# Performance work log

Hardware: AMD Instinct MI355X
Metric: run time of the kernel (lower is better)

## Reference

```python
import jax, jax.numpy as jnp
import numpy as np

NUM_LEVELS = 16
MIN_RES = 16
GROWTH = 1.38
TABLE_SZ = 16384
# Per-level resolutions computed in float64 like torch's python-float b**level
RESOLUTIONS = jnp.asarray(np.floor(MIN_RES * GROWTH ** np.arange(NUM_LEVELS)).astype(np.float32))
# Spatial-hash constants; 2654435761 wraps to int32 like torch's .int() arithmetic
H2 = np.uint32(2654435761).astype(np.int32)
H3 = np.int32(805459861)
# Corner order v0..v7 from get_nearest_vertices_coords: 1 -> use ceil, 0 -> use floor
CORNERS = np.array([[0,0,0],[1,0,0],[1,1,0],[0,1,0],[0,0,1],[1,0,1],[1,1,1],[0,1,1]], dtype=bool)


def setup_inputs() -> dict:
    key = jax.random.key(0)
    kx, kt = jax.random.split(key)
    x = jax.random.uniform(kx, (262144, 3), dtype=jnp.float32)
    # original init: uniform(-1e-4, 1e-4); small-scale random values
    tables = jax.random.normal(kt, (NUM_LEVELS, TABLE_SZ, 2), dtype=jnp.float32) * 1e-4
    return {"x": x, "tables": tables}


def reference(x, tables):
    B = x.shape[0]
    F = tables.shape[-1]
    mask = jnp.asarray(CORNERS)  # [8,3]
    scaled = RESOLUTIONS[:, None, None] * x[None]        # [L,B,3]
    lo = jnp.floor(scaled).astype(jnp.int32)             # [L,B,3]
    hi = jnp.ceil(scaled).astype(jnp.int32)              # [L,B,3]
    verts = jnp.where(mask[None, None], hi[:, :, None, :], lo[:, :, None, :])  # [L,B,8,3]
    vx, vy, vz = verts[..., 0], verts[..., 1], verts[..., 2]
    # int32 spatial hash with wraparound multiply, then python-style mod (non-negative)
    idx = jnp.remainder(vx ^ (H2 * vy) ^ (H3 * vz), TABLE_SZ)  # [L,B,8]
    feats = jax.vmap(lambda t, i: t[i])(tables, idx)           # [L,B,8,F]
    # NOTE: faithful to source: interpolation weights use the UNSCALED position
    w = x - jnp.floor(x)                                       # [B,3]
    # trilinear weight per corner = prod_d (w_d if corner high else 1-w_d)
    cw = jnp.prod(jnp.where(mask[None], w[:, None, :], 1.0 - w[:, None, :]), axis=-1)  # [B,8]
    out = jnp.einsum('lbvf,bv->lbf', feats, cw)                # [L,B,F]
    return jnp.transpose(out, (1, 0, 2)).reshape(B, NUM_LEVELS * F)
```

## Files before the change

### kernel.cpp

```cpp
#include <hip/hip_runtime.h>
#include <hip/hip_fp16.h>
#include <stdint.h>


#define NUM_LEVELS 16
#define TABLE_SZ   16384
#define NCHUNK     32
#define BLOCK      1024

__constant__ float RESV[NUM_LEVELS] = {
    16.f, 22.f, 30.f, 42.f, 58.f, 80.f, 110.f, 152.f,
    210.f, 290.f, 400.f, 553.f, 763.f, 1053.f, 1453.f, 2005.f
};

#define H2_LO 14769u
#define H3_LO 6037u

#define COMPUTE(PX,PY,PZ, OXY0,OXY1,OXY2,OXY3,MZL,MZH, W0,W1,W2,W3,OZ,WZ)      \
    {                                                                          \
        float wx_ = (PX) - floorf(PX);                                         \
        float wy_ = (PY) - floorf(PY);                                         \
        float wz_ = (PZ) - floorf(PZ);                                         \
        float ox_ = 1.f - wx_, oy_ = 1.f - wy_;                                \
        OZ = 1.f - wz_; WZ = wz_;                                              \
        W0 = ox_ * oy_; W1 = wx_ * oy_; W2 = wx_ * wy_; W3 = ox_ * wy_;        \
        float sx_ = r * (PX), sy_ = r * (PY), sz_ = r * (PZ);                  \
        uint32_t mxl_ = ((uint32_t)(int)floorf(sx_) & (TABLE_SZ - 1)) << 2;    \
        uint32_t mxh_ = ((uint32_t)(int)ceilf(sx_)  & (TABLE_SZ - 1)) << 2;    \
        uint32_t myl_ = (__umul24(H2_LO, (uint32_t)(int)floorf(sy_))           \
                         & (TABLE_SZ - 1)) << 2;                               \
        uint32_t myh_ = (__umul24(H2_LO, (uint32_t)(int)ceilf(sy_))            \
                         & (TABLE_SZ - 1)) << 2;                               \
        MZL = (__umul24(H3_LO, (uint32_t)(int)floorf(sz_))                     \
               & (TABLE_SZ - 1)) << 2;                                         \
        MZH = (__umul24(H3_LO, (uint32_t)(int)ceilf(sz_))                      \
               & (TABLE_SZ - 1)) << 2;                                         \
        OXY0 = mxl_ ^ myl_; OXY1 = mxh_ ^ myl_;                                \
        OXY2 = mxh_ ^ myh_; OXY3 = mxl_ ^ myh_;                                \
    }

__global__ __launch_bounds__(BLOCK, 8)
void hashenc_lds_kernel(const float* __restrict__ x,
                        const float* __restrict__ tables,
                        float* __restrict__ out,
                        int B, int pts_per_block)
{
    __shared__ __half2 tab[TABLE_SZ];

    const int level = blockIdx.x >> 5;
    const int chunk = blockIdx.x & (NCHUNK - 1);

    {
        const float4* __restrict__ gt4 =
            (const float4*)(tables + (size_t)level * (TABLE_SZ * 2));
        #pragma unroll
        for (int i = threadIdx.x; i < TABLE_SZ / 2; i += BLOCK) {
            float4 v = gt4[i];
            tab[2 * i]     = __floats2half2_rn(v.x, v.y);
            tab[2 * i + 1] = __floats2half2_rn(v.z, v.w);
        }
    }
    __syncthreads();

    const float r = RESV[level];
    const int b0 = chunk * pts_per_block + threadIdx.x;
    const int iters = pts_per_block / BLOCK;

    const float* __restrict__ xp = x + 3 * (size_t)b0;
    const float* __restrict__ xf = xp + 3 * 2 * BLOCK;
    float2* __restrict__ op = (float2*)out + (size_t)b0 * NUM_LEVELS + level;
    const char* tb = (const char*)tab;

    float px = xp[0], py = xp[1], pz = xp[2];
    uint32_t c_oxy0, c_oxy1, c_oxy2, c_oxy3, c_mzl, c_mzh;
    float    c_w0, c_w1, c_w2, c_w3, c_oz, c_wz;
    COMPUTE(px, py, pz, c_oxy0, c_oxy1, c_oxy2, c_oxy3, c_mzl, c_mzh,
            c_w0, c_w1, c_w2, c_w3, c_oz, c_wz);

    float nx = px, ny = py, nz = pz;
    if (iters > 1) {
        nx = xp[3 * BLOCK + 0];
        ny = xp[3 * BLOCK + 1];
        nz = xp[3 * BLOCK + 2];
    }

    #pragma unroll 1
    for (int k = 0; k < iters; ++k) {
        __half2 h0 = *(const __half2*)(tb + (c_oxy0 ^ c_mzl));
        __half2 h1 = *(const __half2*)(tb + (c_oxy1 ^ c_mzl));
        __half2 h2 = *(const __half2*)(tb + (c_oxy2 ^ c_mzl));
        __half2 h3 = *(const __half2*)(tb + (c_oxy3 ^ c_mzl));
        __half2 h4 = *(const __half2*)(tb + (c_oxy0 ^ c_mzh));
        __half2 h5 = *(const __half2*)(tb + (c_oxy1 ^ c_mzh));
        __half2 h6 = *(const __half2*)(tb + (c_oxy2 ^ c_mzh));
        __half2 h7 = *(const __half2*)(tb + (c_oxy3 ^ c_mzh));

        float fx = nx, fy = ny, fz = nz;
        if (k + 2 < iters) {
            nx = xf[0]; ny = xf[1]; nz = xf[2];
        }
        xf += 3 * BLOCK;

        uint32_t n_oxy0, n_oxy1, n_oxy2, n_oxy3, n_mzl, n_mzh;
        float    n_w0, n_w1, n_w2, n_w3, n_oz, n_wz;
        COMPUTE(fx, fy, fz, n_oxy0, n_oxy1, n_oxy2, n_oxy3, n_mzl, n_mzh,
                n_w0, n_w1, n_w2, n_w3, n_oz, n_wz);

        float a0 = 0.f, a1 = 0.f;
        {
            float w0 = c_w0 * c_oz, w1 = c_w1 * c_oz,
                  w2 = c_w2 * c_oz, w3 = c_w3 * c_oz;
            a0 = fmaf(__low2float(h0),  w0, a0);
            a1 = fmaf(__high2float(h0), w0, a1);
            a0 = fmaf(__low2float(h1),  w1, a0);
            a1 = fmaf(__high2float(h1), w1, a1);
            a0 = fmaf(__low2float(h2),  w2, a0);
            a1 = fmaf(__high2float(h2), w2, a1);
            a0 = fmaf(__low2float(h3),  w3, a0);
            a1 = fmaf(__high2float(h3), w3, a1);
        }
        {
            float w0 = c_w0 * c_wz, w1 = c_w1 * c_wz,
                  w2 = c_w2 * c_wz, w3 = c_w3 * c_wz;
            a0 = fmaf(__low2float(h4),  w0, a0);
            a1 = fmaf(__high2float(h4), w0, a1);
            a0 = fmaf(__low2float(h5),  w1, a0);
            a1 = fmaf(__high2float(h5), w1, a1);
            a0 = fmaf(__low2float(h6),  w2, a0);
            a1 = fmaf(__high2float(h6), w2, a1);
            a0 = fmaf(__low2float(h7),  w3, a0);
            a1 = fmaf(__high2float(h7), w3, a1);
        }

        *op = make_float2(a0, a1);
        op += (size_t)BLOCK * NUM_LEVELS;

        c_oxy0 = n_oxy0; c_oxy1 = n_oxy1; c_oxy2 = n_oxy2; c_oxy3 = n_oxy3;
        c_mzl = n_mzl; c_mzh = n_mzh;
        c_w0 = n_w0; c_w1 = n_w1; c_w2 = n_w2; c_w3 = n_w3;
        c_oz = n_oz; c_wz = n_wz;
    }
}

extern "C" void kernel_launch(void* const* d_in, const int* in_sizes, int n_in,
                              void* d_out, int out_size, void* d_ws, size_t ws_size,
                              hipStream_t stream) {
    const float* x      = (const float*)d_in[0];
    const float* tables = (const float*)d_in[1];
    float* out          = (float*)d_out;
    int B = in_sizes[0] / 3;
    int pts_per_block = (B + NCHUNK - 1) / NCHUNK;
    dim3 grid(NUM_LEVELS * NCHUNK);
    hashenc_lds_kernel<<<grid, BLOCK, 0, stream>>>(x, tables, out, B, pts_per_block);
}
```

Baseline: 88.75 us.

## Deepen software pipeline so LDS gathers overlap previous point's interpolation

Restructures the per-thread loop into a three-stage pipeline: the LDS gathers for the next point are issued before the FMAs that consume the previous point's gathered features, with coordinate prefetch two points ahead. The aim is to hide LDS latency behind arithmetic. It also relaxes launch bounds from 8 to 4 waves per EU, giving more registers for the extra live state while signalling lower occupancy. Since each block uses 64KB LDS with 1024 threads, actual occupancy is likely already bounded by LDS, so the register relaxation mainly avoids spills.

```diff
diff --git a/kernel.cpp b/kernel.cpp
--- a/kernel.cpp
+++ b/kernel.cpp
@@ -39,7 +39,43 @@
         OXY2 = mxh_ ^ myh_; OXY3 = mxl_ ^ myh_;                                \
     }
 
-__global__ __launch_bounds__(BLOCK, 8)
+#define ISSUE(H0,H1,H2,H3,H4,H5,H6,H7, OXY0,OXY1,OXY2,OXY3,MZL,MZH)            \
+    {                                                                          \
+        H0 = *(const __half2*)(tb + ((OXY0) ^ (MZL)));                         \
+        H1 = *(const __half2*)(tb + ((OXY1) ^ (MZL)));                         \
+        H2 = *(const __half2*)(tb + ((OXY2) ^ (MZL)));                         \
+        H3 = *(const __half2*)(tb + ((OXY3) ^ (MZL)));                         \
+        H4 = *(const __half2*)(tb + ((OXY0) ^ (MZH)));                         \
+        H5 = *(const __half2*)(tb + ((OXY1) ^ (MZH)));                         \
+        H6 = *(const __half2*)(tb + ((OXY2) ^ (MZH)));                         \
+        H7 = *(const __half2*)(tb + ((OXY3) ^ (MZH)));                         \
+    }
+
+#define CONSUME(H0,H1,H2,H3,H4,H5,H6,H7, W0,W1,W2,W3,OZ,WZ, A0,A1)             \
+    {                                                                          \
+        float q0 = (W0) * (OZ), q1 = (W1) * (OZ),                              \
+              q2 = (W2) * (OZ), q3 = (W3) * (OZ);                              \
+        A0 = fmaf(__low2float(H0),  q0, A0);                                   \
+        A1 = fmaf(__high2float(H0), q0, A1);                                   \
+        A0 = fmaf(__low2float(H1),  q1, A0);                                   \
+        A1 = fmaf(__high2float(H1), q1, A1);                                   \
+        A0 = fmaf(__low2float(H2),  q2, A0);                                   \
+        A1 = fmaf(__high2float(H2), q2, A1);                                   \
+        A0 = fmaf(__low2float(H3),  q3, A0);                                   \
+        A1 = fmaf(__high2float(H3), q3, A1);                                   \
+        float p0 = (W0) * (WZ), p1 = (W1) * (WZ),                              \
+              p2 = (W2) * (WZ), p3 = (W3) * (WZ);                              \
+        A0 = fmaf(__low2float(H4),  p0, A0);                                   \
+        A1 = fmaf(__high2float(H4), p0, A1);                                   \
+        A0 = fmaf(__low2float(H5),  p1, A0);                                   \
+        A1 = fmaf(__high2float(H5), p1, A1);                                   \
+        A0 = fmaf(__low2float(H6),  p2, A0);                                   \
+        A1 = fmaf(__high2float(H6), p2, A1);                                   \
+        A0 = fmaf(__low2float(H7),  p3, A0);                                   \
+        A1 = fmaf(__high2float(H7), p3, A1);                                   \
+    }
+
+__global__ __launch_bounds__(BLOCK, 4)
 void hashenc_lds_kernel(const float* __restrict__ x,
                         const float* __restrict__ tables,
                         float* __restrict__ out,
@@ -67,78 +103,68 @@
     const int iters = pts_per_block / BLOCK;
 
     const float* __restrict__ xp = x + 3 * (size_t)b0;
-    const float* __restrict__ xf = xp + 3 * 2 * BLOCK;
+    const float* __restrict__ xf = xp + 3 * (size_t)(3 * BLOCK);
     float2* __restrict__ op = (float2*)out + (size_t)b0 * NUM_LEVELS + level;
+    const size_t opstride = (size_t)BLOCK * NUM_LEVELS;
     const char* tb = (const char*)tab;
 
     float px = xp[0], py = xp[1], pz = xp[2];
-    uint32_t c_oxy0, c_oxy1, c_oxy2, c_oxy3, c_mzl, c_mzh;
-    float    c_w0, c_w1, c_w2, c_w3, c_oz, c_wz;
-    COMPUTE(px, py, pz, c_oxy0, c_oxy1, c_oxy2, c_oxy3, c_mzl, c_mzh,
-            c_w0, c_w1, c_w2, c_w3, c_oz, c_wz);
+    uint32_t t0, t1, t2, t3, t4, t5;
+    float aw0, aw1, aw2, aw3, aoz, awz;
+    COMPUTE(px, py, pz, t0, t1, t2, t3, t4, t5, aw0, aw1, aw2, aw3, aoz, awz);
+    __half2 hp0, hp1, hp2, hp3, hp4, hp5, hp6, hp7;
+    ISSUE(hp0, hp1, hp2, hp3, hp4, hp5, hp6, hp7, t0, t1, t2, t3, t4, t5);
 
-    float nx = px, ny = py, nz = pz;
+    float x1x = px, x1y = py, x1z = pz;
     if (iters > 1) {
-        nx = xp[3 * BLOCK + 0];
-        ny = xp[3 * BLOCK + 1];
-        nz = xp[3 * BLOCK + 2];
+        x1x = xp[3 * BLOCK + 0];
+        x1y = xp[3 * BLOCK + 1];
+        x1z = xp[3 * BLOCK + 2];
+    }
+    uint32_t c0, c1, c2, c3, c4, c5;
+    float cw0, cw1, cw2, cw3, coz, cwz;
+    COMPUTE(x1x, x1y, x1z, c0, c1, c2, c3, c4, c5, cw0, cw1, cw2, cw3, coz, cwz);
+
+    float fx = px, fy = py, fz = pz;
+    if (iters > 2) {
+        fx = xp[6 * BLOCK + 0];
+        fy = xp[6 * BLOCK + 1];
+        fz = xp[6 * BLOCK + 2];
     }
 
-    #pragma unroll 1
-    for (int k = 0; k < iters; ++k) {
-        __half2 h0 = *(const __half2*)(tb + (c_oxy0 ^ c_mzl));
-        __half2 h1 = *(const __half2*)(tb + (c_oxy1 ^ c_mzl));
-        __half2 h2 = *(const __half2*)(tb + (c_oxy2 ^ c_mzl));
-        __half2 h3 = *(const __half2*)(tb + (c_oxy3 ^ c_mzl));
-        __half2 h4 = *(const __half2*)(tb + (c_oxy0 ^ c_mzh));
-        __half2 h5 = *(const __half2*)(tb + (c_oxy1 ^ c_mzh));
-        __half2 h6 = *(const __half2*)(tb + (c_oxy2 ^ c_mzh));
-        __half2 h7 = *(const __half2*)(tb + (c_oxy3 ^ c_mzh));
+    #pragma unroll 2
+    for (int k = 1; k < iters; ++k) {
+        __half2 hc0, hc1, hc2, hc3, hc4, hc5, hc6, hc7;
+        ISSUE(hc0, hc1, hc2, hc3, hc4, hc5, hc6, hc7, c0, c1, c2, c3, c4, c5);
 
-        float fx = nx, fy = ny, fz = nz;
+        float gx = fx, gy = fy, gz = fz;
         if (k + 2 < iters) {
-            nx = xf[0]; ny = xf[1]; nz = xf[2];
+            fx = xf[0]; fy = xf[1]; fz = xf[2];
         }
         xf += 3 * BLOCK;
 
-        uint32_t n_oxy0, n_oxy1, n_oxy2, n_oxy3, n_mzl, n_mzh;
-        float    n_w0, n_w1, n_w2, n_w3, n_oz, n_wz;
-        COMPUTE(fx, fy, fz, n_oxy0, n_oxy1, n_oxy2, n_oxy3, n_mzl, n_mzh,
-                n_w0, n_w1, n_w2, n_w3, n_oz, n_wz);
+        uint32_t n0, n1, n2, n3, n4, n5;
+        float nw0, nw1, nw2, nw3, noz, nwz;
+        COMPUTE(gx, gy, gz, n0, n1, n2, n3, n4, n5, nw0, nw1, nw2, nw3, noz, nwz);
 
         float a0 = 0.f, a1 = 0.f;
-        {
-            float w0 = c_w0 * c_oz, w1 = c_w1 * c_oz,
-                  w2 = c_w2 * c_oz, w3 = c_w3 * c_oz;
-            a0 = fmaf(__low2float(h0),  w0, a0);
-            a1 = fmaf(__high2float(h0), w0, a1);
-            a0 = fmaf(__low2float(h1),  w1, a0);
-            a1 = fmaf(__high2float(h1), w1, a1);
-            a0 = fmaf(__low2float(h2),  w2, a0);
-            a1 = fmaf(__high2float(h2), w2, a1);
-            a0 = fmaf(__low2float(h3),  w3, a0);
-            a1 = fmaf(__high2float(h3), w3, a1);
-        }
-        {
-            float w0 = c_w0 * c_wz, w1 = c_w1 * c_wz,
-                  w2 = c_w2 * c_wz, w3 = c_w3 * c_wz;
-            a0 = fmaf(__low2float(h4),  w0, a0);
-            a1 = fmaf(__high2float(h4), w0, a1);
-            a0 = fmaf(__low2float(h5),  w1, a0);
-            a1 = fmaf(__high2float(h5), w1, a1);
-            a0 = fmaf(__low2float(h6),  w2, a0);
-            a1 = fmaf(__high2float(h6), w2, a1);
-            a0 = fmaf(__low2float(h7),  w3, a0);
-            a1 = fmaf(__high2float(h7), w3, a1);
-        }
+        CONSUME(hp0, hp1, hp2, hp3, hp4, hp5, hp6, hp7,
+                aw0, aw1, aw2, aw3, aoz, awz, a0, a1);
+        *op = make_float2(a0, a1);
+        op += opstride;
 
+        hp0 = hc0; hp1 = hc1; hp2 = hc2; hp3 = hc3;
+        hp4 = hc4; hp5 = hc5; hp6 = hc6; hp7 = hc7;
+        aw0 = cw0; aw1 = cw1; aw2 = cw2; aw3 = cw3; aoz = coz; awz = cwz;
+        c0 = n0; c1 = n1; c2 = n2; c3 = n3; c4 = n4; c5 = n5;
+        cw0 = nw0; cw1 = nw1; cw2 = nw2; cw3 = nw3; coz = noz; cwz = nwz;
+    }
+
+    {
+        float a0 = 0.f, a1 = 0.f;
+        CONSUME(hp0, hp1, hp2, hp3, hp4, hp5, hp6, hp7,
+                aw0, aw1, aw2, aw3, aoz, awz, a0, a1);
         *op = make_float2(a0, a1);
-        op += (size_t)BLOCK * NUM_LEVELS;
-
-        c_oxy0 = n_oxy0; c_oxy1 = n_oxy1; c_oxy2 = n_oxy2; c_oxy3 = n_oxy3;
-        c_mzl = n_mzl; c_mzh = n_mzh;
-        c_w0 = n_w0; c_w1 = n_w1; c_w2 = n_w2; c_w3 = n_w3;
-        c_oz = n_oz; c_wz = n_wz;
     }
 }
 
```

Measured after the change: 88.31 us. About the same (-0.5%).
